# Performance work log

Measured on AMD Instinct MI355X. Metric: run time of the kernel, lower is better.

The kernel has to match this reference:

```python
import jax, jax.numpy as jnp
import numpy as np

ALPHA = 0.2       # leakyrelu negative slope
NEG_INF = -9e15   # mask fill value from the torch code
D_OUT = 64


def setup_inputs() -> dict:
    key = jax.random.key(0)
    k1, k2, k3, k4 = jax.random.split(key, 4)
    N, D_IN = 8192, 512
    h = jax.random.normal(k1, (N, D_IN), dtype=jnp.float32)
    W = jax.random.normal(k2, (D_IN, D_OUT), dtype=jnp.float32) * (1.0 / np.sqrt(D_IN))
    a = jax.random.normal(k3, (2 * D_OUT, 1), dtype=jnp.float32) * 0.1
    randomadj = jax.random.randint(k4, (N, N), 0, 2, dtype=jnp.int32)
    return {"h": h, "W": W, "a": a, "randomadj": randomadj}


def reference(h, W, a, randomadj):
    # Wh: [N, D_OUT]
    Wh = h @ W
    # additive attention scores: e[i,j] = leakyrelu(Wh[i]@a1 + Wh[j]@a2)
    Wh1 = Wh @ a[:D_OUT, :]   # [N, 1]
    Wh2 = Wh @ a[D_OUT:, :]   # [N, 1]
    e = jax.nn.leaky_relu(Wh1 + Wh2.T, negative_slope=ALPHA)  # [N, N]
    masked = jnp.where(randomadj > 0, e, NEG_INF)
    attention = jax.nn.softmax(masked, axis=1)  # dropout skipped (eval mode)
    h_prime = attention @ Wh                    # [N, D_OUT]
    return jax.nn.elu(h_prime)                  # concat=True path
```

## Files before the change

kernel.cpp:

```cpp
#include <hip/hip_runtime.h>
#include <stdint.h>


constexpr int NN = 8192;
constexpr int DIN = 512;
constexpr int DOUT = 64;
constexpr int NSPLIT = 8;
constexpr int JCHUNK = NN / NSPLIT;
constexpr int CTILE = 64;
constexpr int NTILES = JCHUNK / CTILE;

typedef __attribute__((ext_vector_type(4))) float f32x4;
typedef __attribute__((ext_vector_type(8))) short short8;

__device__ __forceinline__ unsigned short f2bf(float x) {
  union { float f; uint32_t u; } v; v.f = x;
  return (unsigned short)((v.u + 0x7fffu + ((v.u >> 16) & 1u)) >> 16);
}

__device__ __forceinline__ int frag_byte(int c, int d) {
  int g = (c >> 2) & 3;
  int i = (c & 3) | (((c >> 4) & 1) << 2);
  return ((c >> 5) << 12) | ((d >> 4) << 10) | (((g << 4) | (d & 15)) << 4) | (i << 1);
}

__global__ __launch_bounds__(256) void k1_wh(
    const float* __restrict__ h, const float* __restrict__ W,
    const float* __restrict__ a, unsigned short* __restrict__ whb,
    float* __restrict__ wh1, float* __restrict__ wh2) {
  const int t = threadIdx.x;
  const int w = t >> 6, lane = t & 63;
  const int r = blockIdx.x * 4 + w;
  const float* hr = h + (size_t)r * DIN;
  const float* Wc = W + lane;
  float a0 = 0.f, a1 = 0.f, a2 = 0.f, a3 = 0.f;
#pragma unroll 4
  for (int k = 0; k < DIN; k += 4) {
    a0 = fmaf(hr[k + 0], Wc[(k + 0) * DOUT], a0);
    a1 = fmaf(hr[k + 1], Wc[(k + 1) * DOUT], a1);
    a2 = fmaf(hr[k + 2], Wc[(k + 2) * DOUT], a2);
    a3 = fmaf(hr[k + 3], Wc[(k + 3) * DOUT], a3);
  }
  float acc = (a0 + a1) + (a2 + a3);
  whb[frag_byte(r, lane) >> 1] = f2bf(acc);
  float d1 = acc * a[lane];
  float d2 = acc * a[DOUT + lane];
#pragma unroll
  for (int m = 32; m >= 1; m >>= 1) {
    d1 += __shfl_xor(d1, m, 64);
    d2 += __shfl_xor(d2, m, 64);
  }
  if (lane == 0) { wh1[r] = d1; wh2[r] = d2; }
}

__global__ __launch_bounds__(256) void k2_attn(
    const int* __restrict__ adj, const unsigned short* __restrict__ whb,
    const float* __restrict__ wh1, const float* __restrict__ wh2,
    float* __restrict__ pacc, float* __restrict__ pl) {
  __shared__ char p_frag[8192];
  __shared__ char v_frag[8192];
  __shared__ float lred[256];
  const int t = threadIdx.x;
  const int w = t >> 6, lane = t & 63;
  const int rb = blockIdx.x, sp = blockIdx.y;
  const int r0 = rb * 64;
  const int jbase = sp * JCHUNK;
  const int rloc = t >> 2;
  const int cq = t & 3;
  const float wh1r = wh1[r0 + rloc];
  float lacc = 0.f;
  f32x4 acc[4] = {};
  const size_t adjbase = (size_t)(r0 + rloc) * NN + jbase + cq * 16;
  const int pwbase = (w << 11) | ((cq >> 1) << 10) | ((rloc & 15) << 4) | ((cq & 1) << 3);

  for (int tile = 0; tile < NTILES; ++tile) {
    const int jt = jbase + tile * CTILE;
    const uint4* vsrc = (const uint4*)(whb + ((size_t)(jt >> 5) << 11));
    uint4 va = vsrc[t];
    uint4 vb = vsrc[t + 256];
    const int4* ap = (const int4*)(adj + adjbase + (size_t)tile * CTILE);
    int4 A0 = ap[0], A1 = ap[1], A2 = ap[2], A3 = ap[3];
    const float4* w2p = (const float4*)(wh2 + jt + cq * 16);
    float4 F0 = w2p[0], F1 = w2p[1], F2 = w2p[2], F3 = w2p[3];

    unsigned int pk[8];
    {
      const int av[16] = {A0.x, A0.y, A0.z, A0.w, A1.x, A1.y, A1.z, A1.w,
                          A2.x, A2.y, A2.z, A2.w, A3.x, A3.y, A3.z, A3.w};
      const float wv[16] = {F0.x, F0.y, F0.z, F0.w, F1.x, F1.y, F1.z, F1.w,
                            F2.x, F2.y, F2.z, F2.w, F3.x, F3.y, F3.z, F3.w};
#pragma unroll
      for (int u = 0; u < 16; u += 2) {
        float s0 = wh1r + wv[u];
        float s1 = wh1r + wv[u + 1];
        s0 = s0 > 0.f ? s0 : 0.2f * s0;
        s1 = s1 > 0.f ? s1 : 0.2f * s1;
        float p0 = av[u] > 0 ? __expf(s0) : 0.f;
        float p1 = av[u + 1] > 0 ? __expf(s1) : 0.f;
        lacc += p0 + p1;
        pk[u >> 1] = (unsigned)f2bf(p0) | ((unsigned)f2bf(p1) << 16);
      }
    }
    __syncthreads();
#pragma unroll
    for (int qq = 0; qq < 4; ++qq) {
      uint2 val; val.x = pk[qq * 2]; val.y = pk[qq * 2 + 1];
      *(uint2*)(p_frag + (pwbase | (qq << 8))) = val;
    }
    *(uint4*)(v_frag + t * 16) = va;
    *(uint4*)(v_frag + t * 16 + 4096) = vb;
    __syncthreads();
    short8 af0 = *(const short8*)(p_frag + (w << 11) + (lane << 4));
    short8 af1 = *(const short8*)(p_frag + (w << 11) + 1024 + (lane << 4));
#pragma unroll
    for (int n = 0; n < 4; ++n) {
      short8 b0 = *(const short8*)(v_frag + (n << 10) + (lane << 4));
      short8 b1 = *(const short8*)(v_frag + 4096 + (n << 10) + (lane << 4));
      acc[n] = __builtin_amdgcn_mfma_f32_16x16x32_bf16(af0, b0, acc[n], 0, 0, 0);
      acc[n] = __builtin_amdgcn_mfma_f32_16x16x32_bf16(af1, b1, acc[n], 0, 0, 0);
    }
  }
  lred[t] = lacc;
  __syncthreads();
  if (t < 64) {
    float l = lred[t * 4] + lred[t * 4 + 1] + lred[t * 4 + 2] + lred[t * 4 + 3];
    pl[(size_t)sp * NN + r0 + t] = l;
  }
  float* pa = pacc + (size_t)sp * (NN * DOUT);
#pragma unroll
  for (int n = 0; n < 4; ++n) {
#pragma unroll
    for (int j = 0; j < 4; ++j) {
      int row = r0 + w * 16 + ((lane >> 4) << 2) + j;
      int col = (n << 4) | (lane & 15);
      pa[(size_t)row * DOUT + col] = acc[n][j];
    }
  }
}

__global__ __launch_bounds__(256) void k3_out(
    const float* __restrict__ pacc, const float* __restrict__ pl,
    float* __restrict__ out) {
  const int idx = blockIdx.x * 256 + threadIdx.x;
  const int r = idx >> 6;
  float a = 0.f, l = 0.f;
#pragma unroll
  for (int sp = 0; sp < NSPLIT; ++sp) {
    a += pacc[(size_t)sp * (NN * DOUT) + idx];
    l += pl[(size_t)sp * NN + r];
  }
  float hp = a / l;
  out[idx] = hp > 0.f ? hp : (expf(hp) - 1.f);
}

extern "C" void kernel_launch(void* const* d_in, const int* in_sizes, int n_in,
                              void* d_out, int out_size, void* d_ws, size_t ws_size,
                              hipStream_t stream) {
  const float* h = (const float*)d_in[0];
  const float* W = (const float*)d_in[1];
  const float* a = (const float*)d_in[2];
  const int* adj = (const int*)d_in[3];
  float* out = (float*)d_out;
  char* ws = (char*)d_ws;
  unsigned short* whb = (unsigned short*)ws;
  float* wh1 = (float*)(ws + (1 << 20));
  float* wh2 = (float*)(ws + (1 << 20) + (32 << 10));
  float* pl  = (float*)(ws + (1 << 20) + (64 << 10));
  float* pacc = (float*)(ws + (1 << 20) + (64 << 10) + (256 << 10));
  k1_wh<<<NN / 4, 256, 0, stream>>>(h, W, a, whb, wh1, wh2);
  dim3 g2(NN / 64, NSPLIT);
  k2_attn<<<g2, 256, 0, stream>>>(adj, whb, wh1, wh2, pacc, pl);
  k3_out<<<(NN * DOUT) / 256, 256, 0, stream>>>(pacc, pl, out);
}
```

Before: 493.9 us.

## Rewrite attention kernel to build MFMA fragments in registers and fuse final reduction

The attention kernel now has each wave compute P fragments directly in registers and feed them to MFMA without going through LDS. V fragments are loaded straight from global memory with double-buffered register prefetch and nontemporal adjacency loads. The split-K partial buffers and the separate output kernel are removed: the four waves' partials are reduced in shared memory and ELU is applied inside the same kernel. The Wh projection kernel also switches to float4 vectorized loads. This removes a kernel launch and the partial-sum round trip through global memory, at the cost of higher register pressure and only 512 blocks of 16 rows.

```diff
diff --git a/kernel.cpp b/kernel.cpp
--- a/kernel.cpp
+++ b/kernel.cpp
@@ -5,13 +5,10 @@
 constexpr int NN = 8192;
 constexpr int DIN = 512;
 constexpr int DOUT = 64;
-constexpr int NSPLIT = 8;
-constexpr int JCHUNK = NN / NSPLIT;
-constexpr int CTILE = 64;
-constexpr int NTILES = JCHUNK / CTILE;
 
 typedef __attribute__((ext_vector_type(4))) float f32x4;
 typedef __attribute__((ext_vector_type(8))) short short8;
+typedef int int32x4 __attribute__((ext_vector_type(4)));
 
 __device__ __forceinline__ unsigned short f2bf(float x) {
   union { float f; uint32_t u; } v; v.f = x;
@@ -28,129 +25,136 @@
     const float* __restrict__ h, const float* __restrict__ W,
     const float* __restrict__ a, unsigned short* __restrict__ whb,
     float* __restrict__ wh1, float* __restrict__ wh2) {
-  const int t = threadIdx.x;
-  const int w = t >> 6, lane = t & 63;
+  const int t = threadIdx.x, w = t >> 6, l = t & 63;
   const int r = blockIdx.x * 4 + w;
-  const float* hr = h + (size_t)r * DIN;
-  const float* Wc = W + lane;
-  float a0 = 0.f, a1 = 0.f, a2 = 0.f, a3 = 0.f;
+  const int q = l >> 4, cg = l & 15;
+  const float* hr = h + (size_t)r * DIN + q * 128;
+  const float* Wp = W + (size_t)(q * 128) * DOUT + cg * 4;
+  float ax = 0.f, ay = 0.f, az = 0.f, aw = 0.f;
 #pragma unroll 4
-  for (int k = 0; k < DIN; k += 4) {
-    a0 = fmaf(hr[k + 0], Wc[(k + 0) * DOUT], a0);
-    a1 = fmaf(hr[k + 1], Wc[(k + 1) * DOUT], a1);
-    a2 = fmaf(hr[k + 2], Wc[(k + 2) * DOUT], a2);
-    a3 = fmaf(hr[k + 3], Wc[(k + 3) * DOUT], a3);
+  for (int kk = 0; kk < 32; ++kk) {
+    float4 h4 = *(const float4*)(hr + kk * 4);
+    const float* wr = Wp + (size_t)kk * 4 * DOUT;
+    float4 w0 = *(const float4*)(wr);
+    float4 w1 = *(const float4*)(wr + DOUT);
+    float4 w2 = *(const float4*)(wr + 2 * DOUT);
+    float4 w3 = *(const float4*)(wr + 3 * DOUT);
+    ax = fmaf(h4.x, w0.x, ax); ay = fmaf(h4.x, w0.y, ay); az = fmaf(h4.x, w0.z, az); aw = fmaf(h4.x, w0.w, aw);
+    ax = fmaf(h4.y, w1.x, ax); ay = fmaf(h4.y, w1.y, ay); az = fmaf(h4.y, w1.z, az); aw = fmaf(h4.y, w1.w, aw);
+    ax = fmaf(h4.z, w2.x, ax); ay = fmaf(h4.z, w2.y, ay); az = fmaf(h4.z, w2.z, az); aw = fmaf(h4.z, w2.w, aw);
+    ax = fmaf(h4.w, w3.x, ax); ay = fmaf(h4.w, w3.y, ay); az = fmaf(h4.w, w3.z, az); aw = fmaf(h4.w, w3.w, aw);
   }
-  float acc = (a0 + a1) + (a2 + a3);
-  whb[frag_byte(r, lane) >> 1] = f2bf(acc);
-  float d1 = acc * a[lane];
-  float d2 = acc * a[DOUT + lane];
+  ax += __shfl_xor(ax, 16, 64); ax += __shfl_xor(ax, 32, 64);
+  ay += __shfl_xor(ay, 16, 64); ay += __shfl_xor(ay, 32, 64);
+  az += __shfl_xor(az, 16, 64); az += __shfl_xor(az, 32, 64);
+  aw += __shfl_xor(aw, 16, 64); aw += __shfl_xor(aw, 32, 64);
+  float4 a1v = *(const float4*)(a + cg * 4);
+  float4 a2v = *(const float4*)(a + DOUT + cg * 4);
+  float d1 = ax * a1v.x + ay * a1v.y + az * a1v.z + aw * a1v.w;
+  float d2 = ax * a2v.x + ay * a2v.y + az * a2v.z + aw * a2v.w;
 #pragma unroll
-  for (int m = 32; m >= 1; m >>= 1) {
-    d1 += __shfl_xor(d1, m, 64);
-    d2 += __shfl_xor(d2, m, 64);
-  }
-  if (lane == 0) { wh1[r] = d1; wh2[r] = d2; }
-}
-
-__global__ __launch_bounds__(256) void k2_attn(
-    const int* __restrict__ adj, const unsigned short* __restrict__ whb,
-    const float* __restrict__ wh1, const float* __restrict__ wh2,
-    float* __restrict__ pacc, float* __restrict__ pl) {
-  __shared__ char p_frag[8192];
-  __shared__ char v_frag[8192];
-  __shared__ float lred[256];
-  const int t = threadIdx.x;
-  const int w = t >> 6, lane = t & 63;
-  const int rb = blockIdx.x, sp = blockIdx.y;
-  const int r0 = rb * 64;
-  const int jbase = sp * JCHUNK;
-  const int rloc = t >> 2;
-  const int cq = t & 3;
-  const float wh1r = wh1[r0 + rloc];
-  float lacc = 0.f;
-  f32x4 acc[4] = {};
-  const size_t adjbase = (size_t)(r0 + rloc) * NN + jbase + cq * 16;
-  const int pwbase = (w << 11) | ((cq >> 1) << 10) | ((rloc & 15) << 4) | ((cq & 1) << 3);
-
-  for (int tile = 0; tile < NTILES; ++tile) {
-    const int jt = jbase + tile * CTILE;
-    const uint4* vsrc = (const uint4*)(whb + ((size_t)(jt >> 5) << 11));
-    uint4 va = vsrc[t];
-    uint4 vb = vsrc[t + 256];
-    const int4* ap = (const int4*)(adj + adjbase + (size_t)tile * CTILE);
-    int4 A0 = ap[0], A1 = ap[1], A2 = ap[2], A3 = ap[3];
-    const float4* w2p = (const float4*)(wh2 + jt + cq * 16);
-    float4 F0 = w2p[0], F1 = w2p[1], F2 = w2p[2], F3 = w2p[3];
-
-    unsigned int pk[8];
-    {
-      const int av[16] = {A0.x, A0.y, A0.z, A0.w, A1.x, A1.y, A1.z, A1.w,
-                          A2.x, A2.y, A2.z, A2.w, A3.x, A3.y, A3.z, A3.w};
-      const float wv[16] = {F0.x, F0.y, F0.z, F0.w, F1.x, F1.y, F1.z, F1.w,
-                            F2.x, F2.y, F2.z, F2.w, F3.x, F3.y, F3.z, F3.w};
-#pragma unroll
-      for (int u = 0; u < 16; u += 2) {
-        float s0 = wh1r + wv[u];
-        float s1 = wh1r + wv[u + 1];
-        s0 = s0 > 0.f ? s0 : 0.2f * s0;
-        s1 = s1 > 0.f ? s1 : 0.2f * s1;
-        float p0 = av[u] > 0 ? __expf(s0) : 0.f;
-        float p1 = av[u + 1] > 0 ? __expf(s1) : 0.f;
-        lacc += p0 + p1;
-        pk[u >> 1] = (unsigned)f2bf(p0) | ((unsigned)f2bf(p1) << 16);
-      }
-    }
-    __syncthreads();
-#pragma unroll
-    for (int qq = 0; qq < 4; ++qq) {
-      uint2 val; val.x = pk[qq * 2]; val.y = pk[qq * 2 + 1];
-      *(uint2*)(p_frag + (pwbase | (qq << 8))) = val;
-    }
-    *(uint4*)(v_frag + t * 16) = va;
-    *(uint4*)(v_frag + t * 16 + 4096) = vb;
-    __syncthreads();
-    short8 af0 = *(const short8*)(p_frag + (w << 11) + (lane << 4));
-    short8 af1 = *(const short8*)(p_frag + (w << 11) + 1024 + (lane << 4));
-#pragma unroll
-    for (int n = 0; n < 4; ++n) {
-      short8 b0 = *(const short8*)(v_frag + (n << 10) + (lane << 4));
-      short8 b1 = *(const short8*)(v_frag + 4096 + (n << 10) + (lane << 4));
-      acc[n] = __builtin_amdgcn_mfma_f32_16x16x32_bf16(af0, b0, acc[n], 0, 0, 0);
-      acc[n] = __builtin_amdgcn_mfma_f32_16x16x32_bf16(af1, b1, acc[n], 0, 0, 0);
-    }
-  }
-  lred[t] = lacc;
-  __syncthreads();
-  if (t < 64) {
-    float l = lred[t * 4] + lred[t * 4 + 1] + lred[t * 4 + 2] + lred[t * 4 + 3];
-    pl[(size_t)sp * NN + r0 + t] = l;
-  }
-  float* pa = pacc + (size_t)sp * (NN * DOUT);
-#pragma unroll
-  for (int n = 0; n < 4; ++n) {
-#pragma unroll
-    for (int j = 0; j < 4; ++j) {
-      int row = r0 + w * 16 + ((lane >> 4) << 2) + j;
-      int col = (n << 4) | (lane & 15);
-      pa[(size_t)row * DOUT + col] = acc[n][j];
-    }
+  for (int m = 8; m >= 1; m >>= 1) { d1 += __shfl_xor(d1, m, 64); d2 += __shfl_xor(d2, m, 64); }
+  if (l == 0) { wh1[r] = d1; wh2[r] = d2; }
+  if (l < 16) {
+    whb[frag_byte(r, cg * 4 + 0) >> 1] = f2bf(ax);
+    whb[frag_byte(r, cg * 4 + 1) >> 1] = f2bf(ay);
+    whb[frag_byte(r, cg * 4 + 2) >> 1] = f2bf(az);
+    whb[frag_byte(r, cg * 4 + 3) >> 1] = f2bf(aw);
   }
 }
 
-__global__ __launch_bounds__(256) void k3_out(
-    const float* __restrict__ pacc, const float* __restrict__ pl,
+struct KRegs {
+  int32x4 a0, a1;
+  float4 f0, f1;
+  uint4 v0, v1, v2, v3;
+};
+
+__global__ __launch_bounds__(256, 2) void k2_attn(
+    const int* __restrict__ adj, const unsigned short* __restrict__ whb,
+    const float* __restrict__ wh1, const float* __restrict__ wh2,
     float* __restrict__ out) {
-  const int idx = blockIdx.x * 256 + threadIdx.x;
-  const int r = idx >> 6;
-  float a = 0.f, l = 0.f;
-#pragma unroll
-  for (int sp = 0; sp < NSPLIT; ++sp) {
-    a += pacc[(size_t)sp * (NN * DOUT) + idx];
-    l += pl[(size_t)sp * NN + r];
+  __shared__ float accs[4][16][64];
+  __shared__ float lsum[4][16];
+  const int t = threadIdx.x, w = t >> 6, l = t & 63;
+  const int r0 = blockIdx.x * 16;
+  const int row = l & 15, g = l >> 4;
+  const float wh1r = wh1[r0 + row];
+  const int jb = w * 2048 + 4 * g;
+  const int32x4* adjp = (const int32x4*)(adj + (size_t)(r0 + row) * NN + jb);
+  const float4* w2p = (const float4*)(wh2 + jb);
+  const uint4* vp = (const uint4*)whb + (size_t)w * 64 * 256 + l;
+  f32x4 acc0 = {}, acc1 = {}, acc2 = {}, acc3 = {};
+  float lacc = 0.f;
+
+#define LOADC(R, c) do { \
+    R.a0 = __builtin_nontemporal_load(adjp + (c) * 8); \
+    R.a1 = __builtin_nontemporal_load(adjp + (c) * 8 + 4); \
+    R.f0 = w2p[(c) * 8]; R.f1 = w2p[(c) * 8 + 4]; \
+    R.v0 = vp[(c) * 256]; R.v1 = vp[(c) * 256 + 64]; \
+    R.v2 = vp[(c) * 256 + 128]; R.v3 = vp[(c) * 256 + 192]; \
+  } while (0)
+
+#define SC(pv, av, fv) { float s_ = wh1r + (fv); s_ = fmaxf(s_, 0.2f * s_); \
+                         float e_ = __expf(s_); pv = ((av) > 0) ? e_ : 0.f; }
+
+#define COMP(R) do { \
+    float p0, p1, p2, p3, p4, p5, p6, p7; \
+    SC(p0, R.a0.x, R.f0.x) SC(p1, R.a0.y, R.f0.y) SC(p2, R.a0.z, R.f0.z) SC(p3, R.a0.w, R.f0.w) \
+    SC(p4, R.a1.x, R.f1.x) SC(p5, R.a1.y, R.f1.y) SC(p6, R.a1.z, R.f1.z) SC(p7, R.a1.w, R.f1.w) \
+    lacc += ((p0 + p1) + (p2 + p3)) + ((p4 + p5) + (p6 + p7)); \
+    union { uint32_t u[4]; short8 s; } af; \
+    af.u[0] = f2bf(p0) | ((uint32_t)f2bf(p1) << 16); \
+    af.u[1] = f2bf(p2) | ((uint32_t)f2bf(p3) << 16); \
+    af.u[2] = f2bf(p4) | ((uint32_t)f2bf(p5) << 16); \
+    af.u[3] = f2bf(p6) | ((uint32_t)f2bf(p7) << 16); \
+    union { uint4 q; short8 s; } b0, b1, b2, b3; \
+    b0.q = R.v0; b1.q = R.v1; b2.q = R.v2; b3.q = R.v3; \
+    acc0 = __builtin_amdgcn_mfma_f32_16x16x32_bf16(af.s, b0.s, acc0, 0, 0, 0); \
+    acc1 = __builtin_amdgcn_mfma_f32_16x16x32_bf16(af.s, b1.s, acc1, 0, 0, 0); \
+    acc2 = __builtin_amdgcn_mfma_f32_16x16x32_bf16(af.s, b2.s, acc2, 0, 0, 0); \
+    acc3 = __builtin_amdgcn_mfma_f32_16x16x32_bf16(af.s, b3.s, acc3, 0, 0, 0); \
+  } while (0)
+
+  KRegs A, B;
+  LOADC(A, 0);
+  LOADC(B, 1);
+  for (int c = 0; c + 2 < 64; c += 2) {
+    COMP(A); LOADC(A, c + 2);
+    COMP(B); LOADC(B, c + 3);
   }
-  float hp = a / l;
-  out[idx] = hp > 0.f ? hp : (expf(hp) - 1.f);
+  COMP(A);
+  COMP(B);
+
+  lacc += __shfl_xor(lacc, 16, 64);
+  lacc += __shfl_xor(lacc, 32, 64);
+  if (l < 16) lsum[w][l] = lacc;
+  {
+    const int rb = (l >> 4) * 4, cl = l & 15;
+#define WACC(an, n) { accs[w][rb + 0][(n)*16 + cl] = an[0]; accs[w][rb + 1][(n)*16 + cl] = an[1]; \
+                      accs[w][rb + 2][(n)*16 + cl] = an[2]; accs[w][rb + 3][(n)*16 + cl] = an[3]; }
+    WACC(acc0, 0) WACC(acc1, 1) WACC(acc2, 2) WACC(acc3, 3)
+#undef WACC
+  }
+  __syncthreads();
+  {
+    const int rr = t >> 4, dq = (t & 15) * 4;
+    float4 s0 = *(const float4*)&accs[0][rr][dq];
+    float4 s1 = *(const float4*)&accs[1][rr][dq];
+    float4 s2 = *(const float4*)&accs[2][rr][dq];
+    float4 s3 = *(const float4*)&accs[3][rr][dq];
+    float L = (lsum[0][rr] + lsum[1][rr]) + (lsum[2][rr] + lsum[3][rr]);
+    float inv = 1.0f / L;
+    float4 o;
+    float v;
+    v = (s0.x + s1.x + s2.x + s3.x) * inv; o.x = v > 0.f ? v : __expf(v) - 1.f;
+    v = (s0.y + s1.y + s2.y + s3.y) * inv; o.y = v > 0.f ? v : __expf(v) - 1.f;
+    v = (s0.z + s1.z + s2.z + s3.z) * inv; o.z = v > 0.f ? v : __expf(v) - 1.f;
+    v = (s0.w + s1.w + s2.w + s3.w) * inv; o.w = v > 0.f ? v : __expf(v) - 1.f;
+    *(float4*)(out + (size_t)(r0 + rr) * DOUT + dq) = o;
+  }
+#undef LOADC
+#undef SC
+#undef COMP
 }
 
 extern "C" void kernel_launch(void* const* d_in, const int* in_sizes, int n_in,
@@ -165,10 +169,6 @@
   unsigned short* whb = (unsigned short*)ws;
   float* wh1 = (float*)(ws + (1 << 20));
   float* wh2 = (float*)(ws + (1 << 20) + (32 << 10));
-  float* pl  = (float*)(ws + (1 << 20) + (64 << 10));
-  float* pacc = (float*)(ws + (1 << 20) + (64 << 10) + (256 << 10));
   k1_wh<<<NN / 4, 256, 0, stream>>>(h, W, a, whb, wh1, wh2);
-  dim3 g2(NN / 64, NSPLIT);
-  k2_attn<<<g2, 256, 0, stream>>>(adj, whb, wh1, wh2, pacc, pl);
-  k3_out<<<(NN * DOUT) / 256, 256, 0, stream>>>(pacc, pl, out);
+  k2_attn<<<NN / 16, 256, 0, stream>>>(adj, whb, wh1, wh2, out);
 }
```

Result: faster. 433.3 us (-12.3%).
